# Kernel tuning notes

Hardware: AMD Instinct MI355X
Metric: run time of the kernel (lower is better)

Reference implementation:

```python
import jax, jax.numpy as jnp
import numpy as np

N_NODES = 100000


def _gcn_norm(edge_index, n):
    # PyG GCNConv default: add self-loops, symmetric normalization
    src, dst = edge_index[0], edge_index[1]
    loops = jnp.arange(n, dtype=src.dtype)
    src = jnp.concatenate([src, loops])
    dst = jnp.concatenate([dst, loops])
    deg = jax.ops.segment_sum(jnp.ones_like(dst, dtype=jnp.float32), dst, num_segments=n)
    dinv = jnp.where(deg > 0, jax.lax.rsqrt(deg), 0.0)
    norm = dinv[src] * dinv[dst]  # [E+N]
    return src, dst, norm


def _gcn_conv(x, src, dst, norm, W, b, n):
    h = x @ W                                  # [N, out] transform first
    msg = h[src] * norm[:, None]               # gather + edge weight
    out = jax.ops.segment_sum(msg, dst, num_segments=n)  # scatter-add
    return out + b


def setup_inputs() -> dict:
    key = jax.random.key(0)
    k1, k2, k3, k4 = jax.random.split(key, 4)
    in_f, h_f, out_f = 128, 256, 128
    x = jax.random.normal(k1, (N_NODES, in_f), dtype=jnp.float32)
    edge_index = jax.random.randint(k2, (2, 1600000), 0, N_NODES, dtype=jnp.int64)
    W1 = jax.random.normal(k3, (in_f, h_f), dtype=jnp.float32) / np.sqrt(in_f)
    b1 = jnp.zeros((h_f,), dtype=jnp.float32)
    W2 = jax.random.normal(k4, (h_f, out_f), dtype=jnp.float32) / np.sqrt(h_f)
    b2 = jnp.zeros((out_f,), dtype=jnp.float32)
    return {"x": x, "edge_index": edge_index, "W1": W1, "b1": b1, "W2": W2, "b2": b2}


def reference(x, edge_index, W1, b1, W2, b2):
    n = x.shape[0]
    src, dst, norm = _gcn_norm(edge_index, n)
    h = jax.nn.relu(_gcn_conv(x, src, dst, norm, W1, b1, n))
    return _gcn_conv(h, src, dst, norm, W2, b2, n)
```

## Files before the change

### kernel.cpp

```cpp
#include <hip/hip_runtime.h>

typedef __bf16 bf16x8 __attribute__((ext_vector_type(8)));
typedef float f32x4 __attribute__((ext_vector_type(4)));

#define DEVI static __device__ __forceinline__
#define CHUNK 4096
#define SCH 8192

DEVI unsigned short f2bf(float f){
  unsigned int x = __builtin_bit_cast(unsigned int, f);
  x = (x + 0x7fffu + ((x >> 16) & 1u)) >> 16;
  return (unsigned short)x;
}
DEVI unsigned int packbf2(float a, float b){
  return (unsigned int)f2bf(a) | ((unsigned int)f2bf(b) << 16);
}
DEVI float bflo(unsigned int u){ return __builtin_bit_cast(float, u << 16); }
DEVI float bfhi(unsigned int u){ return __builtin_bit_cast(float, u & 0xffff0000u); }

__global__ void k_zero(int* __restrict__ p, int n){
  int i = blockIdx.x*256 + threadIdx.x;
  if (i < n) p[i] = 0;
}


__global__ __launch_bounds__(256) void kb_hist(const int* __restrict__ dst,
    int* __restrict__ bucketCnt, int E, int NB){
  __shared__ int h[2048];
  for (int i=threadIdx.x;i<NB;i+=256) h[i]=0;
  __syncthreads();
  int base = blockIdx.x*CHUNK;
  int lim = base+CHUNK < E ? base+CHUNK : E;
  for (int i = base+threadIdx.x; i < lim; i += 256)
    atomicAdd(&h[dst[i]>>8], 1);
  __syncthreads();
  for (int i=threadIdx.x;i<NB;i+=256)
    if (h[i]) atomicAdd(&bucketCnt[i], h[i]);
}

__global__ __launch_bounds__(256) void kb_scan(const int* __restrict__ bucketCnt,
    int* __restrict__ bucketOff, int* __restrict__ bucketCur,
    int* __restrict__ cCur, int NB, int NBC){
  __shared__ int sh[256];
  int t = threadIdx.x;
  int per = (NB+255)/256;
  int vals[8];
  int lsum = 0;
  for (int j=0;j<per;j++){
    int i = t*per+j;
    int v = (i<NB) ? bucketCnt[i] : 0;
    vals[j]=v; lsum+=v;
  }
  sh[t]=lsum; __syncthreads();
  for (int off=1; off<256; off<<=1){
    int x = (t>=off) ? sh[t-off] : 0;
    __syncthreads();
    sh[t] += x;
    __syncthreads();
  }
  int run = sh[t]-lsum;
  for (int j=0;j<per;j++){
    int i = t*per+j;
    if (i<NB){ bucketOff[i]=run; bucketCur[i]=run; }
    run += vals[j];
  }
  if (t==255) bucketOff[NB]=run;
  __syncthreads();
  for (int c=t;c<NBC;c+=256){
    int f = c*8;
    cCur[c] = bucketOff[f < NB ? f : NB];
  }
}

__global__ __launch_bounds__(512) void kb_scat1(const int* __restrict__ src,
    const int* __restrict__ dst, int* __restrict__ cur,
    int* __restrict__ srco, int* __restrict__ dsto, int E, int NBK){
  __shared__ int h[64];
  __shared__ int baseSh[64];
  int t = threadIdx.x;
  if (t < NBK){ h[t]=0; }
  __syncthreads();
  int base = blockIdx.x*SCH;
  int lim = base+SCH < E ? base+SCH : E;
  for (int i = base+t; i < lim; i += 512)
    atomicAdd(&h[dst[i]>>11], 1);
  __syncthreads();
  if (t < NBK){
    int c = h[t];
    baseSh[t] = c ? atomicAdd(&cur[t], c) : 0;
    h[t] = 0;
  }
  __syncthreads();
  for (int i = base+t; i < lim; i += 512){
    int d = dst[i];
    int b = d>>11;
    int r = atomicAdd(&h[b], 1);
    int p = baseSh[b] + r;
    srco[p] = src[i];
    dsto[p] = d;
  }
}

__global__ __launch_bounds__(512) void kb_scat2(const int* __restrict__ src,
    const int* __restrict__ dst, int* __restrict__ cur,
    int* __restrict__ pk, int E, int NBK){
  __shared__ int h[2048];
  __shared__ int baseSh[2048];
  int t = threadIdx.x;
  for (int i=t;i<NBK;i+=512) h[i]=0;
  __syncthreads();
  int base = blockIdx.x*SCH;
  int lim = base+SCH < E ? base+SCH : E;
  for (int i = base+t; i < lim; i += 512)
    atomicAdd(&h[dst[i]>>8], 1);
  __syncthreads();
  for (int i=t;i<NBK;i+=512){
    int c = h[i];
    baseSh[i] = c ? atomicAdd(&cur[i], c) : 0;
    h[i] = 0;
  }
  __syncthreads();
  for (int i = base+t; i < lim; i += 512){
    int d = dst[i];
    int b = d>>8;
    int r = atomicAdd(&h[b], 1);
    int p = baseSh[b] + r;
    pk[p] = (src[i]<<8) | (d&255);
  }
}

__global__ __launch_bounds__(256) void kb_fused(const int* __restrict__ pk,
    const int* __restrict__ bOff,
    int* __restrict__ rp, int* __restrict__ csr, float* __restrict__ dinv,
    int n, int NB, int E){
  __shared__ int c[256];
  __shared__ int sh[256];
  __shared__ int cur[256];
  int t = threadIdx.x;
  int b = blockIdx.x;
  int s = bOff[b], e2 = bOff[b+1];
  c[t]=0; __syncthreads();
  for (int i=s+t;i<e2;i+=256) atomicAdd(&c[pk[i]&255], 1);
  __syncthreads();
  int deg = c[t];
  sh[t]=deg; __syncthreads();
  for (int o=1;o<256;o<<=1){
    int x = (t>=o) ? sh[t-o] : 0;
    __syncthreads();
    sh[t]+=x;
    __syncthreads();
  }
  int excl = sh[t]-deg;
  int node = b*256+t;
  if (node<n){
    rp[node] = s + excl;
    dinv[node] = rsqrtf((float)(deg+1));
  }
  if (b==NB-1 && t==0) rp[n] = E;
  cur[t] = s + excl;
  __syncthreads();
  for (int i=s+t;i<e2;i+=256){
    int p = pk[i];
    int r = atomicAdd(&cur[p&255], 1);
    csr[r] = p & (int)0xFFFFFF00u;
  }
}

DEVI void packW(const float* __restrict__ W, unsigned short* __restrict__ Wp,
                int idx, int N, int NF){
  int l = idx & 63;
  int frag = idx >> 6;
  int cf = frag % NF;
  int ks = frag / NF;
  int kbase = ks*32 + (l>>4)*8;
  int col = cf*16 + (l&15);
  unsigned short* dp = Wp + (size_t)idx*8;
  #pragma unroll
  for (int j=0;j<8;j++) dp[j] = f2bf(W[(size_t)(kbase+j)*N + col]);
}

__global__ void k_prep(const float2* __restrict__ x, const float* __restrict__ dinv,
                       unsigned int* __restrict__ xb, int n2, int NCVT,
                       const float* __restrict__ W1, unsigned short* __restrict__ W1p,
                       const float* __restrict__ W2, unsigned short* __restrict__ W2p){
  int blk = blockIdx.x;
  if (blk < NCVT){
    int i = blk*256 + threadIdx.x;
    if (i<n2){
      float d = dinv[i>>6];
      float2 v = x[i];
      xb[i] = packbf2(d*v.x, d*v.y);
    }
  } else {
    int idx = (blk-NCVT)*256 + threadIdx.x;
    if (idx < 4096) packW(W1, W1p, idx, 256, 16);
    else            packW(W2, W2p, idx-4096, 128, 8);
  }
}

#define ACC8(V) { a0+=bflo(V.x); a1+=bfhi(V.x); a2+=bflo(V.y); a3+=bfhi(V.y); \
                  a4+=bflo(V.z); a5+=bfhi(V.z); a6+=bflo(V.w); a7+=bfhi(V.w); }

template<bool FINAL>
__global__ __launch_bounds__(256) void k_agg(
    const unsigned int* __restrict__ xs, const int* __restrict__ rp,
    const int* __restrict__ csr, const float* __restrict__ dinv,
    const float* __restrict__ bias, unsigned int* __restrict__ outb,
    float* __restrict__ outf, int n){
  int node = blockIdx.x*4 + (threadIdx.x>>6);
  if (node >= n) return;
  int l = threadIdx.x & 63;
  int q = l & 15;
  int h = l >> 4;
  const char* xbase = (const char*)xs;
  float a0=0,a1=0,a2=0,a3=0,a4=0,a5=0,a6=0,a7=0;
  int e = rp[node], end = rp[node+1];
  int p = e;
  int nf = (end - e) >> 4;
  for (int blk=0; blk<nf; ++blk, p+=16){
    uint4 v[4];
    #pragma unroll
    for (int i=0;i<4;i++){
      int boff = csr[p + 4*i + h];
      v[i] = *(const uint4*)(xbase + (size_t)(unsigned)boff + q*16);
    }
    ACC8(v[0]); ACC8(v[1]); ACC8(v[2]); ACC8(v[3]);
  }
  int rem = end - p;
  if (rem >= 8){
    uint4 v[2];
    #pragma unroll
    for (int i=0;i<2;i++){
      int boff = csr[p + 4*i + h];
      v[i] = *(const uint4*)(xbase + (size_t)(unsigned)boff + q*16);
    }
    ACC8(v[0]); ACC8(v[1]);
    p += 8; rem -= 8;
  }
  if (rem > 0){
    uint4 v[2];
    #pragma unroll
    for (int i=0;i<2;i++){
      int ei = p + 4*i + h;
      int ec = ei < end-1 ? ei : end-1;
      int boff = csr[ec];
      uint4 t = *(const uint4*)(xbase + (size_t)(unsigned)boff + q*16);
      if (ei >= end){ t.x=0; t.y=0; t.z=0; t.w=0; }
      v[i] = t;
    }
    ACC8(v[0]); ACC8(v[1]);
  }
  a0 += __shfl_xor(a0,16); a0 += __shfl_xor(a0,32);
  a1 += __shfl_xor(a1,16); a1 += __shfl_xor(a1,32);
  a2 += __shfl_xor(a2,16); a2 += __shfl_xor(a2,32);
  a3 += __shfl_xor(a3,16); a3 += __shfl_xor(a3,32);
  a4 += __shfl_xor(a4,16); a4 += __shfl_xor(a4,32);
  a5 += __shfl_xor(a5,16); a5 += __shfl_xor(a5,32);
  a6 += __shfl_xor(a6,16); a6 += __shfl_xor(a6,32);
  a7 += __shfl_xor(a7,16); a7 += __shfl_xor(a7,32);
  uint4 sv = *(const uint4*)(xbase + (size_t)node*256 + q*16);
  ACC8(sv);
  float dn = dinv[node];
  if constexpr (FINAL){
    if (h < 2){
      const float4 bb = *(const float4*)(bias + 8*q + 4*h);
      f32x4 r;
      r.x = (h ? a4 : a0)*dn + bb.x;
      r.y = (h ? a5 : a1)*dn + bb.y;
      r.z = (h ? a6 : a2)*dn + bb.z;
      r.w = (h ? a7 : a3)*dn + bb.w;
      __builtin_nontemporal_store(r, (f32x4*)(outf + (size_t)node*128 + 8*q + 4*h));
    }
  } else {
    if (h == 0){
      uint4 o;
      o.x = packbf2(a0*dn, a1*dn);
      o.y = packbf2(a2*dn, a3*dn);
      o.z = packbf2(a4*dn, a5*dn);
      o.w = packbf2(a6*dn, a7*dn);
      *(uint4*)((char*)outb + (size_t)node*256 + q*16) = o;
    }
  }
}

template<int K, int N, bool BIASRELU, bool ROWSCALE>
__global__ __launch_bounds__(256) void k_gemm(
    const unsigned short* __restrict__ A, const unsigned short* __restrict__ Wp,
    const float* __restrict__ bias, const float* __restrict__ rowscale,
    unsigned short* __restrict__ C, int M){
  constexpr int KS = K/32;
  constexpr int NF = N/16;
  constexpr int NWC = N/64;
  constexpr int NWR = 4/NWC;
  constexpr int BM = 64*NWR;
  int l = threadIdx.x & 63;
  int w = threadIdx.x >> 6;
  int wr = w / NWC, wc = w % NWC;
  int r0 = blockIdx.x*BM + wr*64;
  int c0 = wc*64;
  int lr = l & 15, lg = l >> 4;
  f32x4 acc[4][4];
  #pragma unroll
  for (int i=0;i<4;i++)
    #pragma unroll
    for (int j=0;j<4;j++)
      acc[i][j] = f32x4{0.f,0.f,0.f,0.f};
  for (int ks=0; ks<KS; ++ks){
    bf16x8 a[4], b[4];
    #pragma unroll
    for (int ar=0;ar<4;ar++){
      int row = r0 + ar*16 + lr;
      if (row > M-1) row = M-1;
      const uint4* p = (const uint4*)(A + (size_t)row*K + ks*32 + lg*8);
      union { uint4 u; bf16x8 v; } t; t.u = *p; a[ar] = t.v;
    }
    #pragma unroll
    for (int cb=0;cb<4;cb++){
      int cf = (c0>>4) + cb;
      const uint4* p = (const uint4*)(Wp + ((size_t)(ks*NF + cf)*64 + l)*8);
      union { uint4 u; bf16x8 v; } t; t.u = *p; b[cb] = t.v;
    }
    #pragma unroll
    for (int ar=0;ar<4;ar++)
      #pragma unroll
      for (int cb=0;cb<4;cb++)
        acc[ar][cb] = __builtin_amdgcn_mfma_f32_16x16x32_bf16(a[ar], b[cb], acc[ar][cb], 0, 0, 0);
  }
  #pragma unroll
  for (int ar=0;ar<4;ar++){
    #pragma unroll
    for (int i=0;i<4;i++){
      int row = r0 + ar*16 + lg*4 + i;
      if (row < M){
        float rs = 1.f;
        if constexpr (ROWSCALE) rs = rowscale[row];
        #pragma unroll
        for (int cb=0;cb<4;cb++){
          int col = c0 + cb*16 + lr;
          float v = acc[ar][cb][i];
          if constexpr (BIASRELU){ v += bias[col]; v = fmaxf(v, 0.f); }
          if constexpr (ROWSCALE) v *= rs;
          C[(size_t)row*N + col] = f2bf(v);
        }
      }
    }
  }
}

extern "C" void kernel_launch(void* const* d_in, const int* in_sizes, int n_in,
                              void* d_out, int out_size, void* d_ws, size_t ws_size,
                              hipStream_t stream){
  const float* x  = (const float*)d_in[0];
  const int*   ei = (const int*)d_in[1];
  const float* W1 = (const float*)d_in[2];
  const float* b1 = (const float*)d_in[3];
  const float* W2 = (const float*)d_in[4];
  const float* b2 = (const float*)d_in[5];
  const int IN_F = 128, H_F = 256, OUT_F = 128;
  int n = in_sizes[0] / IN_F;
  int E = in_sizes[1] / 2;
  const int* srcI = ei;
  const int* dstI = ei + E;
  const int NB  = (n+255)>>8;
  const int NBC = (n+2047)>>11;

  char* ws = (char*)d_ws;
  size_t off = 0;
  auto alloc = [&](size_t bytes)->char*{
    char* p = ws + off; off += (bytes + 255) & ~(size_t)255; return p;
  };
  int*   rp    = (int*)  alloc(((size_t)n+1)*4);
  float* dinv  = (float*)alloc((size_t)n*4);
  int*   bCnt  = (int*)  alloc((size_t)NB*4);
  int*   bOff  = (int*)  alloc(((size_t)NB+1)*4);
  int*   bCur  = (int*)  alloc((size_t)NB*4);
  int*   cCur  = (int*)  alloc(((size_t)NBC+1)*4);
  unsigned short* W1p = (unsigned short*)alloc((size_t)IN_F*H_F*2);
  unsigned short* W2p = (unsigned short*)alloc((size_t)H_F*OUT_F*2);
  int*   csr   = (int*)  alloc((size_t)E*4);
  unsigned int* xb = (unsigned int*)alloc((size_t)n*(IN_F/2)*4);
  unsigned int* AX = (unsigned int*)alloc((size_t)n*(IN_F/2)*4);
  unsigned short* H1 = (unsigned short*)alloc((size_t)n*H_F*2);
  int* srcc = (int*)H1;
  int* dstc = srcc + E;
  int* pk   = dstc + E;

  int NCH = (E + CHUNK - 1)/CHUNK;
  int NSC = (E + SCH - 1)/SCH;
  int NCVT = (n*(IN_F/2) + 255)/256;

  k_zero<<<(NB+255)/256,256,0,stream>>>(bCnt, NB);
  kb_hist<<<NCH,256,0,stream>>>(dstI, bCnt, E, NB);
  kb_scan<<<1,256,0,stream>>>(bCnt, bOff, bCur, cCur, NB, NBC);
  kb_scat1<<<NSC,512,0,stream>>>(srcI, dstI, cCur, srcc, dstc, E, NBC);
  kb_scat2<<<NSC,512,0,stream>>>(srcc, dstc, bCur, pk, E, NB);
  kb_fused<<<NB,256,0,stream>>>(pk, bOff, rp, csr, dinv, n, NB, E);
  k_prep<<<NCVT+32,256,0,stream>>>((const float2*)x, dinv, xb, n*(IN_F/2), NCVT,
                                   W1, W1p, W2, W2p);
  k_agg<false><<<(n+3)/4,256,0,stream>>>(xb, rp, csr, dinv, nullptr, AX, nullptr, n);
  k_gemm<128,256,true,false><<<(n+63)/64,256,0,stream>>>((const unsigned short*)AX, W1p, b1, nullptr, H1, n);
  unsigned int* T = xb;
  k_gemm<256,128,false,true><<<(n+127)/128,256,0,stream>>>(H1, W2p, nullptr, dinv, (unsigned short*)T, n);
  k_agg<true><<<(n+3)/4,256,0,stream>>>(T, rp, csr, dinv, b2, nullptr, (float*)d_out, n);
}
```

Before: 276.3 us.

## Fuse layer-1 aggregation with GEMM and fold x conversion into CSR build

Merges the first-layer neighbor aggregation into the first GEMM. Each block aggregates 64 nodes into a swizzled LDS tile and then runs the MFMA GEMM straight from LDS, so the AX intermediate is never written to or read from global memory. The x-to-bf16 conversion (scaled by dinv) and the weight packing move into the CSR-building kernel, which removes one launch and one dinv reload. In exchange, the aggregation now runs 16 nodes per wave serially inside fewer blocks, which may reduce parallelism for latency-bound gathers.

```diff
diff --git a/kernel.cpp b/kernel.cpp
--- a/kernel.cpp
+++ b/kernel.cpp
@@ -129,43 +129,6 @@
   }
 }
 
-__global__ __launch_bounds__(256) void kb_fused(const int* __restrict__ pk,
-    const int* __restrict__ bOff,
-    int* __restrict__ rp, int* __restrict__ csr, float* __restrict__ dinv,
-    int n, int NB, int E){
-  __shared__ int c[256];
-  __shared__ int sh[256];
-  __shared__ int cur[256];
-  int t = threadIdx.x;
-  int b = blockIdx.x;
-  int s = bOff[b], e2 = bOff[b+1];
-  c[t]=0; __syncthreads();
-  for (int i=s+t;i<e2;i+=256) atomicAdd(&c[pk[i]&255], 1);
-  __syncthreads();
-  int deg = c[t];
-  sh[t]=deg; __syncthreads();
-  for (int o=1;o<256;o<<=1){
-    int x = (t>=o) ? sh[t-o] : 0;
-    __syncthreads();
-    sh[t]+=x;
-    __syncthreads();
-  }
-  int excl = sh[t]-deg;
-  int node = b*256+t;
-  if (node<n){
-    rp[node] = s + excl;
-    dinv[node] = rsqrtf((float)(deg+1));
-  }
-  if (b==NB-1 && t==0) rp[n] = E;
-  cur[t] = s + excl;
-  __syncthreads();
-  for (int i=s+t;i<e2;i+=256){
-    int p = pk[i];
-    int r = atomicAdd(&cur[p&255], 1);
-    csr[r] = p & (int)0xFFFFFF00u;
-  }
-}
-
 DEVI void packW(const float* __restrict__ W, unsigned short* __restrict__ Wp,
                 int idx, int N, int NF){
   int l = idx & 63;
@@ -179,34 +142,198 @@
   for (int j=0;j<8;j++) dp[j] = f2bf(W[(size_t)(kbase+j)*N + col]);
 }
 
-__global__ void k_prep(const float2* __restrict__ x, const float* __restrict__ dinv,
-                       unsigned int* __restrict__ xb, int n2, int NCVT,
-                       const float* __restrict__ W1, unsigned short* __restrict__ W1p,
-                       const float* __restrict__ W2, unsigned short* __restrict__ W2p){
-  int blk = blockIdx.x;
-  if (blk < NCVT){
-    int i = blk*256 + threadIdx.x;
-    if (i<n2){
-      float d = dinv[i>>6];
-      float2 v = x[i];
-      xb[i] = packbf2(d*v.x, d*v.y);
-    }
-  } else {
-    int idx = (blk-NCVT)*256 + threadIdx.x;
+__global__ __launch_bounds__(256) void kb_fused(const int* __restrict__ pk,
+    const int* __restrict__ bOff,
+    int* __restrict__ rp, int* __restrict__ csr, float* __restrict__ dinv,
+    const float2* __restrict__ x2, unsigned int* __restrict__ xb,
+    const float* __restrict__ W1, unsigned short* __restrict__ W1p,
+    const float* __restrict__ W2, unsigned short* __restrict__ W2p,
+    int n, int NB, int E){
+  int t = threadIdx.x;
+  int b = blockIdx.x;
+  if (b >= NB){
+    int idx = (b-NB)*256 + t;
     if (idx < 4096) packW(W1, W1p, idx, 256, 16);
     else            packW(W2, W2p, idx-4096, 128, 8);
+    return;
+  }
+  __shared__ int c[256];
+  __shared__ int sh[256];
+  __shared__ int cur[256];
+  __shared__ float dv[256];
+  int s = bOff[b], e2 = bOff[b+1];
+  c[t]=0; __syncthreads();
+  for (int i=s+t;i<e2;i+=256) atomicAdd(&c[pk[i]&255], 1);
+  __syncthreads();
+  int deg = c[t];
+  sh[t]=deg; __syncthreads();
+  for (int o=1;o<256;o<<=1){
+    int x = (t>=o) ? sh[t-o] : 0;
+    __syncthreads();
+    sh[t]+=x;
+    __syncthreads();
+  }
+  int excl = sh[t]-deg;
+  int node = b*256+t;
+  float dnv = rsqrtf((float)(deg+1));
+  if (node<n){
+    rp[node] = s + excl;
+    dinv[node] = dnv;
+  }
+  if (b==NB-1 && t==0) rp[n] = E;
+  cur[t] = s + excl;
+  dv[t] = dnv;
+  __syncthreads();
+  for (int i=s+t;i<e2;i+=256){
+    int p = pk[i];
+    int r = atomicAdd(&cur[p&255], 1);
+    csr[r] = p & (int)0xFFFFFF00u;
+  }
+  int base_node = b*256;
+  int rows = n - base_node; if (rows > 256) rows = 256;
+  int j = t & 63;
+  for (int rb = t>>6; rb < rows; rb += 4){
+    int nd = base_node + rb;
+    float d = dv[rb];
+    float2 v = x2[(size_t)nd*64 + j];
+    xb[(size_t)nd*64 + j] = packbf2(d*v.x, d*v.y);
   }
 }
 
 #define ACC8(V) { a0+=bflo(V.x); a1+=bfhi(V.x); a2+=bflo(V.y); a3+=bfhi(V.y); \
                   a4+=bflo(V.z); a5+=bfhi(V.z); a6+=bflo(V.w); a7+=bfhi(V.w); }
 
-template<bool FINAL>
-__global__ __launch_bounds__(256) void k_agg(
+DEVI int lds_g(int row, int g){ return row*256 + (((g & 8) | ((g & 7) ^ (row & 7)))<<4); }
+
+__global__ __launch_bounds__(256) void k_aggemm1(
     const unsigned int* __restrict__ xs, const int* __restrict__ rp,
     const int* __restrict__ csr, const float* __restrict__ dinv,
-    const float* __restrict__ bias, unsigned int* __restrict__ outb,
-    float* __restrict__ outf, int n){
+    const unsigned short* __restrict__ Wp, const float* __restrict__ bias,
+    unsigned short* __restrict__ C, int n){
+  __shared__ unsigned char At[64*256];
+  int l = threadIdx.x & 63;
+  int w = threadIdx.x >> 6;
+  int r0 = blockIdx.x*64;
+  int q = l & 15;
+  int h = l >> 4;
+  const char* xbase = (const char*)xs;
+  for (int nn=0; nn<16; ++nn){
+    int row = w*16 + nn;
+    int node = r0 + row;
+    float a0=0,a1=0,a2=0,a3=0,a4=0,a5=0,a6=0,a7=0;
+    float dn = 0.f;
+    if (node < n){
+      int e = rp[node], end = rp[node+1];
+      int p = e;
+      int nf = (end - e) >> 4;
+      for (int blk=0; blk<nf; ++blk, p+=16){
+        uint4 v[4];
+        #pragma unroll
+        for (int i=0;i<4;i++){
+          int boff = csr[p + 4*i + h];
+          v[i] = *(const uint4*)(xbase + (size_t)(unsigned)boff + q*16);
+        }
+        ACC8(v[0]); ACC8(v[1]); ACC8(v[2]); ACC8(v[3]);
+      }
+      int rem = end - p;
+      if (rem >= 8){
+        uint4 v[2];
+        #pragma unroll
+        for (int i=0;i<2;i++){
+          int boff = csr[p + 4*i + h];
+          v[i] = *(const uint4*)(xbase + (size_t)(unsigned)boff + q*16);
+        }
+        ACC8(v[0]); ACC8(v[1]);
+        p += 8; rem -= 8;
+      }
+      if (rem > 0){
+        uint4 v[2];
+        #pragma unroll
+        for (int i=0;i<2;i++){
+          int ei = p + 4*i + h;
+          int ec = ei < end-1 ? ei : end-1;
+          int boff = csr[ec];
+          uint4 tv = *(const uint4*)(xbase + (size_t)(unsigned)boff + q*16);
+          if (ei >= end){ tv.x=0; tv.y=0; tv.z=0; tv.w=0; }
+          v[i] = tv;
+        }
+        ACC8(v[0]); ACC8(v[1]);
+      }
+      a0 += __shfl_xor(a0,16); a0 += __shfl_xor(a0,32);
+      a1 += __shfl_xor(a1,16); a1 += __shfl_xor(a1,32);
+      a2 += __shfl_xor(a2,16); a2 += __shfl_xor(a2,32);
+      a3 += __shfl_xor(a3,16); a3 += __shfl_xor(a3,32);
+      a4 += __shfl_xor(a4,16); a4 += __shfl_xor(a4,32);
+      a5 += __shfl_xor(a5,16); a5 += __shfl_xor(a5,32);
+      a6 += __shfl_xor(a6,16); a6 += __shfl_xor(a6,32);
+      a7 += __shfl_xor(a7,16); a7 += __shfl_xor(a7,32);
+      uint4 sv = *(const uint4*)(xbase + (size_t)node*256 + q*16);
+      ACC8(sv);
+      dn = dinv[node];
+    }
+    if (h == 0){
+      uint4 o;
+      o.x = packbf2(a0*dn, a1*dn);
+      o.y = packbf2(a2*dn, a3*dn);
+      o.z = packbf2(a4*dn, a5*dn);
+      o.w = packbf2(a6*dn, a7*dn);
+      *(uint4*)(At + lds_g(row, q)) = o;
+    }
+  }
+  __syncthreads();
+  int lr = l & 15, lg = l >> 4;
+  int c0 = w*64;
+  f32x4 acc[4][4];
+  #pragma unroll
+  for (int i=0;i<4;i++)
+    #pragma unroll
+    for (int j2=0;j2<4;j2++)
+      acc[i][j2] = f32x4{0.f,0.f,0.f,0.f};
+  #pragma unroll
+  for (int ks=0; ks<4; ++ks){
+    bf16x8 a[4], b[4];
+    #pragma unroll
+    for (int ar=0;ar<4;ar++){
+      int row = ar*16 + lr;
+      int ga = ks*4 + lg;
+      union { uint4 u; bf16x8 v; } t2;
+      t2.u = *(const uint4*)(At + lds_g(row, ga));
+      a[ar] = t2.v;
+    }
+    #pragma unroll
+    for (int cb=0;cb<4;cb++){
+      int cf = (c0>>4) + cb;
+      const uint4* p = (const uint4*)(Wp + ((size_t)(ks*16 + cf)*64 + l)*8);
+      union { uint4 u; bf16x8 v; } t2; t2.u = *p; b[cb] = t2.v;
+    }
+    #pragma unroll
+    for (int ar=0;ar<4;ar++)
+      #pragma unroll
+      for (int cb=0;cb<4;cb++)
+        acc[ar][cb] = __builtin_amdgcn_mfma_f32_16x16x32_bf16(a[ar], b[cb], acc[ar][cb], 0, 0, 0);
+  }
+  #pragma unroll
+  for (int ar=0;ar<4;ar++){
+    #pragma unroll
+    for (int i=0;i<4;i++){
+      int grow = r0 + ar*16 + lg*4 + i;
+      if (grow < n){
+        #pragma unroll
+        for (int cb=0;cb<4;cb++){
+          int col = c0 + cb*16 + lr;
+          float v = acc[ar][cb][i] + bias[col];
+          v = fmaxf(v, 0.f);
+          C[(size_t)grow*256 + col] = f2bf(v);
+        }
+      }
+    }
+  }
+}
+
+__global__ __launch_bounds__(256) void k_agg2(
+    const unsigned int* __restrict__ xs, const int* __restrict__ rp,
+    const int* __restrict__ csr, const float* __restrict__ dinv,
+    const float* __restrict__ bias, float* __restrict__ outf, int n){
   int node = blockIdx.x*4 + (threadIdx.x>>6);
   if (node >= n) return;
   int l = threadIdx.x & 63;
@@ -261,33 +388,21 @@
   uint4 sv = *(const uint4*)(xbase + (size_t)node*256 + q*16);
   ACC8(sv);
   float dn = dinv[node];
-  if constexpr (FINAL){
-    if (h < 2){
-      const float4 bb = *(const float4*)(bias + 8*q + 4*h);
-      f32x4 r;
-      r.x = (h ? a4 : a0)*dn + bb.x;
-      r.y = (h ? a5 : a1)*dn + bb.y;
-      r.z = (h ? a6 : a2)*dn + bb.z;
-      r.w = (h ? a7 : a3)*dn + bb.w;
-      __builtin_nontemporal_store(r, (f32x4*)(outf + (size_t)node*128 + 8*q + 4*h));
-    }
-  } else {
-    if (h == 0){
-      uint4 o;
-      o.x = packbf2(a0*dn, a1*dn);
-      o.y = packbf2(a2*dn, a3*dn);
-      o.z = packbf2(a4*dn, a5*dn);
-      o.w = packbf2(a6*dn, a7*dn);
-      *(uint4*)((char*)outb + (size_t)node*256 + q*16) = o;
-    }
-  }
-}
-
-template<int K, int N, bool BIASRELU, bool ROWSCALE>
-__global__ __launch_bounds__(256) void k_gemm(
+  if (h < 2){
+    const float4 bb = *(const float4*)(bias + 8*q + 4*h);
+    f32x4 r;
+    r.x = (h ? a4 : a0)*dn + bb.x;
+    r.y = (h ? a5 : a1)*dn + bb.y;
+    r.z = (h ? a6 : a2)*dn + bb.z;
+    r.w = (h ? a7 : a3)*dn + bb.w;
+    __builtin_nontemporal_store(r, (f32x4*)(outf + (size_t)node*128 + 8*q + 4*h));
+  }
+}
+
+__global__ __launch_bounds__(256) void k_gemm2(
     const unsigned short* __restrict__ A, const unsigned short* __restrict__ Wp,
-    const float* __restrict__ bias, const float* __restrict__ rowscale,
-    unsigned short* __restrict__ C, int M){
+    const float* __restrict__ rowscale, unsigned short* __restrict__ C, int M){
+  constexpr int K = 256, N = 128;
   constexpr int KS = K/32;
   constexpr int NF = N/16;
   constexpr int NWC = N/64;
@@ -332,15 +447,11 @@
     for (int i=0;i<4;i++){
       int row = r0 + ar*16 + lg*4 + i;
       if (row < M){
-        float rs = 1.f;
-        if constexpr (ROWSCALE) rs = rowscale[row];
+        float rs = rowscale[row];
         #pragma unroll
         for (int cb=0;cb<4;cb++){
           int col = c0 + cb*16 + lr;
-          float v = acc[ar][cb][i];
-          if constexpr (BIASRELU){ v += bias[col]; v = fmaxf(v, 0.f); }
-          if constexpr (ROWSCALE) v *= rs;
-          C[(size_t)row*N + col] = f2bf(v);
+          C[(size_t)row*N + col] = f2bf(acc[ar][cb][i] * rs);
         }
       }
     }
@@ -379,7 +490,6 @@
   unsigned short* W2p = (unsigned short*)alloc((size_t)H_F*OUT_F*2);
   int*   csr   = (int*)  alloc((size_t)E*4);
   unsigned int* xb = (unsigned int*)alloc((size_t)n*(IN_F/2)*4);
-  unsigned int* AX = (unsigned int*)alloc((size_t)n*(IN_F/2)*4);
   unsigned short* H1 = (unsigned short*)alloc((size_t)n*H_F*2);
   int* srcc = (int*)H1;
   int* dstc = srcc + E;
@@ -387,19 +497,16 @@
 
   int NCH = (E + CHUNK - 1)/CHUNK;
   int NSC = (E + SCH - 1)/SCH;
-  int NCVT = (n*(IN_F/2) + 255)/256;
 
   k_zero<<<(NB+255)/256,256,0,stream>>>(bCnt, NB);
   kb_hist<<<NCH,256,0,stream>>>(dstI, bCnt, E, NB);
   kb_scan<<<1,256,0,stream>>>(bCnt, bOff, bCur, cCur, NB, NBC);
   kb_scat1<<<NSC,512,0,stream>>>(srcI, dstI, cCur, srcc, dstc, E, NBC);
   kb_scat2<<<NSC,512,0,stream>>>(srcc, dstc, bCur, pk, E, NB);
-  kb_fused<<<NB,256,0,stream>>>(pk, bOff, rp, csr, dinv, n, NB, E);
-  k_prep<<<NCVT+32,256,0,stream>>>((const float2*)x, dinv, xb, n*(IN_F/2), NCVT,
-                                   W1, W1p, W2, W2p);
-  k_agg<false><<<(n+3)/4,256,0,stream>>>(xb, rp, csr, dinv, nullptr, AX, nullptr, n);
-  k_gemm<128,256,true,false><<<(n+63)/64,256,0,stream>>>((const unsigned short*)AX, W1p, b1, nullptr, H1, n);
+  kb_fused<<<NB+32,256,0,stream>>>(pk, bOff, rp, csr, dinv,
+                                   (const float2*)x, xb, W1, W1p, W2, W2p, n, NB, E);
+  k_aggemm1<<<(n+63)/64,256,0,stream>>>(xb, rp, csr, dinv, W1p, b1, H1, n);
   unsigned int* T = xb;
-  k_gemm<256,128,false,true><<<(n+127)/128,256,0,stream>>>(H1, W2p, nullptr, dinv, (unsigned short*)T, n);
-  k_agg<true><<<(n+3)/4,256,0,stream>>>(T, rp, csr, dinv, b2, nullptr, (float*)d_out, n);
-}
+  k_gemm2<<<(n+127)/128,256,0,stream>>>(H1, W2p, dinv, (unsigned short*)T, n);
+  k_agg2<<<(n+3)/4,256,0,stream>>>(T, rp, csr, dinv, b2, (float*)d_out, n);
+}
```

New measurement: 324.6 us. +17.5%, slower.

## Pack src/dst into one word in the first scatter and fuse x conversion into CSR build

Applied to the files above, without the earlier changes.

The first radix-scatter pass now writes a single packed int (src<<11 | low dst bits) instead of separate src and dst arrays. The second pass no longer rescans all edges. It processes each coarse bucket's contiguous range and splits it into its 8 fine sub-buckets, so it only needs small shared histograms. The x-to-bf16 scaling and weight packing are folded into the CSR-building kernel, which removes one launch and the global dinv reread. These changes cut edge-sort memory traffic and launch count, but src<<11 must still fit in 32 bits and the sub-bucket order within blocks is nondeterministic.

```diff
diff --git a/kernel.cpp b/kernel.cpp
--- a/kernel.cpp
+++ b/kernel.cpp
@@ -74,7 +74,7 @@
 
 __global__ __launch_bounds__(512) void kb_scat1(const int* __restrict__ src,
     const int* __restrict__ dst, int* __restrict__ cur,
-    int* __restrict__ srco, int* __restrict__ dsto, int E, int NBK){
+    int* __restrict__ p1, int E, int NBK){
   __shared__ int h[64];
   __shared__ int baseSh[64];
   int t = threadIdx.x;
@@ -96,73 +96,38 @@
     int b = d>>11;
     int r = atomicAdd(&h[b], 1);
     int p = baseSh[b] + r;
-    srco[p] = src[i];
-    dsto[p] = d;
-  }
-}
-
-__global__ __launch_bounds__(512) void kb_scat2(const int* __restrict__ src,
-    const int* __restrict__ dst, int* __restrict__ cur,
-    int* __restrict__ pk, int E, int NBK){
-  __shared__ int h[2048];
-  __shared__ int baseSh[2048];
+    p1[p] = (src[i]<<11) | (d & 2047);
+  }
+}
+
+__global__ __launch_bounds__(512) void kb_scat2(const int* __restrict__ p1,
+    const int* __restrict__ bOff, int* __restrict__ cur,
+    int* __restrict__ pk, int NB){
+  __shared__ int h[8];
+  __shared__ int baseSh[8];
   int t = threadIdx.x;
-  for (int i=t;i<NBK;i+=512) h[i]=0;
-  __syncthreads();
-  int base = blockIdx.x*SCH;
-  int lim = base+SCH < E ? base+SCH : E;
-  for (int i = base+t; i < lim; i += 512)
-    atomicAdd(&h[dst[i]>>8], 1);
-  __syncthreads();
-  for (int i=t;i<NBK;i+=512){
-    int c = h[i];
-    baseSh[i] = c ? atomicAdd(&cur[i], c) : 0;
-    h[i] = 0;
-  }
-  __syncthreads();
-  for (int i = base+t; i < lim; i += 512){
-    int d = dst[i];
-    int b = d>>8;
-    int r = atomicAdd(&h[b], 1);
-    int p = baseSh[b] + r;
-    pk[p] = (src[i]<<8) | (d&255);
-  }
-}
-
-__global__ __launch_bounds__(256) void kb_fused(const int* __restrict__ pk,
-    const int* __restrict__ bOff,
-    int* __restrict__ rp, int* __restrict__ csr, float* __restrict__ dinv,
-    int n, int NB, int E){
-  __shared__ int c[256];
-  __shared__ int sh[256];
-  __shared__ int cur[256];
-  int t = threadIdx.x;
-  int b = blockIdx.x;
-  int s = bOff[b], e2 = bOff[b+1];
-  c[t]=0; __syncthreads();
-  for (int i=s+t;i<e2;i+=256) atomicAdd(&c[pk[i]&255], 1);
-  __syncthreads();
-  int deg = c[t];
-  sh[t]=deg; __syncthreads();
-  for (int o=1;o<256;o<<=1){
-    int x = (t>=o) ? sh[t-o] : 0;
-    __syncthreads();
-    sh[t]+=x;
-    __syncthreads();
-  }
-  int excl = sh[t]-deg;
-  int node = b*256+t;
-  if (node<n){
-    rp[node] = s + excl;
-    dinv[node] = rsqrtf((float)(deg+1));
-  }
-  if (b==NB-1 && t==0) rp[n] = E;
-  cur[t] = s + excl;
-  __syncthreads();
-  for (int i=s+t;i<e2;i+=256){
-    int p = pk[i];
-    int r = atomicAdd(&cur[p&255], 1);
-    csr[r] = p & (int)0xFFFFFF00u;
+  int bc = blockIdx.x >> 3;
+  int sub = blockIdx.x & 7;
+  int s = bOff[bc*8];
+  int fe = bc*8+8; if (fe > NB) fe = NB;
+  int e = bOff[fe];
+  if (t < 8) h[t] = 0;
+  __syncthreads();
+  for (int i = s + sub*512 + t; i < e; i += 4096)
+    atomicAdd(&h[(p1[i]>>8)&7], 1);
+  __syncthreads();
+  if (t < 8){
+    int c2 = h[t];
+    baseSh[t] = c2 ? atomicAdd(&cur[bc*8+t], c2) : 0;
+    h[t] = 0;
+  }
+  __syncthreads();
+  for (int i = s + sub*512 + t; i < e; i += 4096){
+    int p = p1[i];
+    int f = (p>>8)&7;
+    int r = atomicAdd(&h[f], 1);
+    int pos = baseSh[f] + r;
+    pk[pos] = ((p>>11)<<8) | (p&255);
   }
 }
 
@@ -179,22 +144,61 @@
   for (int j=0;j<8;j++) dp[j] = f2bf(W[(size_t)(kbase+j)*N + col]);
 }
 
-__global__ void k_prep(const float2* __restrict__ x, const float* __restrict__ dinv,
-                       unsigned int* __restrict__ xb, int n2, int NCVT,
-                       const float* __restrict__ W1, unsigned short* __restrict__ W1p,
-                       const float* __restrict__ W2, unsigned short* __restrict__ W2p){
-  int blk = blockIdx.x;
-  if (blk < NCVT){
-    int i = blk*256 + threadIdx.x;
-    if (i<n2){
-      float d = dinv[i>>6];
-      float2 v = x[i];
-      xb[i] = packbf2(d*v.x, d*v.y);
-    }
-  } else {
-    int idx = (blk-NCVT)*256 + threadIdx.x;
+__global__ __launch_bounds__(256) void kb_fused(const int* __restrict__ pk,
+    const int* __restrict__ bOff,
+    int* __restrict__ rp, int* __restrict__ csr, float* __restrict__ dinv,
+    const float2* __restrict__ x2, unsigned int* __restrict__ xb,
+    const float* __restrict__ W1, unsigned short* __restrict__ W1p,
+    const float* __restrict__ W2, unsigned short* __restrict__ W2p,
+    int n, int NB, int E){
+  int t = threadIdx.x;
+  int b = blockIdx.x;
+  if (b >= NB){
+    int idx = (b-NB)*256 + t;
     if (idx < 4096) packW(W1, W1p, idx, 256, 16);
     else            packW(W2, W2p, idx-4096, 128, 8);
+    return;
+  }
+  __shared__ int c[256];
+  __shared__ int sh[256];
+  __shared__ int cur[256];
+  __shared__ float dv[256];
+  int s = bOff[b], e2 = bOff[b+1];
+  c[t]=0; __syncthreads();
+  for (int i=s+t;i<e2;i+=256) atomicAdd(&c[pk[i]&255], 1);
+  __syncthreads();
+  int deg = c[t];
+  sh[t]=deg; __syncthreads();
+  for (int o=1;o<256;o<<=1){
+    int x = (t>=o) ? sh[t-o] : 0;
+    __syncthreads();
+    sh[t]+=x;
+    __syncthreads();
+  }
+  int excl = sh[t]-deg;
+  int node = b*256+t;
+  float dnv = rsqrtf((float)(deg+1));
+  if (node<n){
+    rp[node] = s + excl;
+    dinv[node] = dnv;
+  }
+  if (b==NB-1 && t==0) rp[n] = E;
+  cur[t] = s + excl;
+  dv[t] = dnv;
+  __syncthreads();
+  for (int i=s+t;i<e2;i+=256){
+    int p = pk[i];
+    int r = atomicAdd(&cur[p&255], 1);
+    csr[r] = p & (int)0xFFFFFF00u;
+  }
+  int base_node = b*256;
+  int rows = n - base_node; if (rows > 256) rows = 256;
+  int j = t & 63;
+  for (int rb = t>>6; rb < rows; rb += 4){
+    int nd = base_node + rb;
+    float d = dv[rb];
+    float2 v = x2[(size_t)nd*64 + j];
+    xb[(size_t)nd*64 + j] = packbf2(d*v.x, d*v.y);
   }
 }
 
@@ -381,22 +385,19 @@
   unsigned int* xb = (unsigned int*)alloc((size_t)n*(IN_F/2)*4);
   unsigned int* AX = (unsigned int*)alloc((size_t)n*(IN_F/2)*4);
   unsigned short* H1 = (unsigned short*)alloc((size_t)n*H_F*2);
-  int* srcc = (int*)H1;
-  int* dstc = srcc + E;
-  int* pk   = dstc + E;
+  int* p1 = (int*)H1;
+  int* pk = p1 + E;
 
   int NCH = (E + CHUNK - 1)/CHUNK;
   int NSC = (E + SCH - 1)/SCH;
-  int NCVT = (n*(IN_F/2) + 255)/256;
 
   k_zero<<<(NB+255)/256,256,0,stream>>>(bCnt, NB);
   kb_hist<<<NCH,256,0,stream>>>(dstI, bCnt, E, NB);
   kb_scan<<<1,256,0,stream>>>(bCnt, bOff, bCur, cCur, NB, NBC);
-  kb_scat1<<<NSC,512,0,stream>>>(srcI, dstI, cCur, srcc, dstc, E, NBC);
-  kb_scat2<<<NSC,512,0,stream>>>(srcc, dstc, bCur, pk, E, NB);
-  kb_fused<<<NB,256,0,stream>>>(pk, bOff, rp, csr, dinv, n, NB, E);
-  k_prep<<<NCVT+32,256,0,stream>>>((const float2*)x, dinv, xb, n*(IN_F/2), NCVT,
-                                   W1, W1p, W2, W2p);
+  kb_scat1<<<NSC,512,0,stream>>>(srcI, dstI, cCur, p1, E, NBC);
+  kb_scat2<<<NBC*8,512,0,stream>>>(p1, bOff, bCur, pk, NB);
+  kb_fused<<<NB+32,256,0,stream>>>(pk, bOff, rp, csr, dinv,
+                                   (const float2*)x, xb, W1, W1p, W2, W2p, n, NB, E);
   k_agg<false><<<(n+3)/4,256,0,stream>>>(xb, rp, csr, dinv, nullptr, AX, nullptr, n);
   k_gemm<128,256,true,false><<<(n+63)/64,256,0,stream>>>((const unsigned short*)AX, W1p, b1, nullptr, H1, n);
   unsigned int* T = xb;
```

Result: faster. 261.2 us (-5.5%).
